# Kernel optimization log

Measured on AMD Instinct MI355X. Metric: run time of the kernel, lower is better.

## Reference

```python
import jax, jax.numpy as jnp
import numpy as np

D_MODEL, N_LEVELS, N_HEADS, N_POINTS = 256, 4, 8, 4
DH = D_MODEL // N_HEADS
SPATIAL = np.array([[92, 92], [46, 46], [23, 23], [12, 12]], dtype=np.int64)
LEVEL_START = np.concatenate([[0], np.cumsum(SPATIAL[:, 0] * SPATIAL[:, 1])[:-1]]).astype(np.int64)
LEN_IN = int((SPATIAL[:, 0] * SPATIAL[:, 1]).sum())  # 11253
B, Q = 2, LEN_IN


def _radial_bias():
    # Matches FlashDeformAttnTorch._reset_parameters sampling_offsets bias init.
    thetas = np.arange(N_HEADS, dtype=np.float32) * (2.0 * np.pi / N_HEADS)
    grid = np.stack([np.cos(thetas), np.sin(thetas)], -1)  # (G,2)
    grid = grid / np.abs(grid).max(-1, keepdims=True)
    grid = np.tile(grid[:, None, None, :], (1, N_LEVELS, N_POINTS, 1)).copy()
    for i in range(N_POINTS):
        grid[:, :, i, :] *= i + 1
    return jnp.asarray(grid.reshape(-1), dtype=jnp.float32)


def setup_inputs() -> dict:
    key = jax.random.key(0)
    ks = jax.random.split(key, 10)
    s = 1.0 / np.sqrt(D_MODEL)
    return {
        "query": jax.random.normal(ks[0], (B, Q, D_MODEL), jnp.float32),
        "reference_points": jax.random.uniform(ks[1], (B, Q, N_LEVELS, 2), jnp.float32),
        "input_flatten": jax.random.normal(ks[2], (B, LEN_IN, D_MODEL), jnp.float32),
        "spatial_shapes": SPATIAL,
        "level_start_index": LEVEL_START,
        "W_off": jax.random.normal(ks[3], (D_MODEL, N_HEADS * N_LEVELS * N_POINTS * 2), jnp.float32) * 0.01,
        "b_off": _radial_bias(),
        "W_attn": jax.random.normal(ks[4], (D_MODEL, N_HEADS * N_LEVELS * N_POINTS), jnp.float32) * 0.01,
        "b_attn": jnp.zeros((N_HEADS * N_LEVELS * N_POINTS,), jnp.float32),
        "W_val": jax.random.normal(ks[5], (D_MODEL, D_MODEL), jnp.float32) * s,
        "b_val": jnp.zeros((D_MODEL,), jnp.float32),
        "W_out": jax.random.normal(ks[6], (D_MODEL, D_MODEL), jnp.float32) * s,
        "b_out": jnp.zeros((D_MODEL,), jnp.float32),
    }


def _forward(query, reference_points, input_flatten, W_off, b_off, W_attn, b_attn,
             W_val, b_val, W_out, b_out, spatial_shapes, level_start_index):
    Bn, Qn, _ = query.shape
    G, L, K, Dh = N_HEADS, N_LEVELS, N_POINTS, DH
    ss = np.asarray(spatial_shapes)
    lsi = np.asarray(level_start_index)

    value = (input_flatten @ W_val + b_val).reshape(Bn, -1, G, Dh)
    offsets = (query @ W_off + b_off).reshape(Bn, Qn, G, L, K, 2)
    logits = (query @ W_attn + b_attn).reshape(Bn, Qn, G, L * K)
    attn = jax.nn.softmax(logits, axis=-1).reshape(Bn, Qn, G, L, K)

    # normalizer stacks (W, H) per level
    normalizer = jnp.asarray(np.stack([ss[:, 1], ss[:, 0]], -1).astype(np.float32))
    loc = reference_points[:, :, None, :, None, :] + offsets / normalizer[None, None, None, :, None, :]
    # loc: (B, Q, G, L, K, 2) with (..., 0)=x, (..., 1)=y in [0,1]

    out = jnp.zeros((Bn, Qn, G, Dh), value.dtype)
    for lvl in range(L):
        H, W = int(ss[lvl, 0]), int(ss[lvl, 1])
        start = int(lsi[lvl])
        vlev = value[:, start:start + H * W].transpose(0, 2, 1, 3)  # (B, G, H*W, Dh)
        h_im = loc[:, :, :, lvl, :, 1] * H - 0.5  # (B, Q, G, K)
        w_im = loc[:, :, :, lvl, :, 0] * W - 0.5
        h0 = jnp.floor(h_im); w0 = jnp.floor(w_im)
        lh = h_im - h0; lw = w_im - w0
        hh = 1.0 - lh; hw = 1.0 - lw
        h0i = h0.astype(jnp.int32); w0i = w0.astype(jnp.int32)

        def corner(hi, wi, vlev=vlev, H=H, W=W):
            m = (hi >= 0) & (hi < H) & (wi >= 0) & (wi < W)
            idx = jnp.clip(hi, 0, H - 1) * W + jnp.clip(wi, 0, W - 1)  # (B,Q,G,K)
            idx_bg = idx.transpose(0, 2, 1, 3).reshape(Bn, G, Qn * K)
            g = jax.vmap(jax.vmap(lambda v, i: v[i]))(vlev, idx_bg)  # (B,G,Q*K,Dh)
            g = g.reshape(Bn, G, Qn, K, Dh).transpose(0, 2, 1, 3, 4)  # (B,Q,G,K,Dh)
            return g * m.transpose(0, 1, 2, 3)[..., None].astype(g.dtype)

        v1 = corner(h0i, w0i)
        v2 = corner(h0i, w0i + 1)
        v3 = corner(h0i + 1, w0i)
        v4 = corner(h0i + 1, w0i + 1)
        sampled = (v1 * (hh * hw)[..., None] + v2 * (hh * lw)[..., None]
                   + v3 * (lh * hw)[..., None] + v4 * (lh * lw)[..., None])
        valid = (h_im > -1) & (w_im > -1) & (h_im < H) & (w_im < W)
        sampled = sampled * valid[..., None].astype(sampled.dtype)
        out = out + (sampled * attn[:, :, :, lvl, :, None]).sum(axis=3)

    out = out.reshape(Bn, Qn, G * Dh)
    return out @ W_out + b_out


def reference(query, reference_points, input_flatten, spatial_shapes, level_start_index,
              W_off, b_off, W_attn, b_attn, W_val, b_val, W_out, b_out):
    return _forward(query, reference_points, input_flatten, W_off, b_off, W_attn, b_attn,
                    W_val, b_val, W_out, b_out, spatial_shapes, level_start_index)
```

## Files before the change

### kernel.cpp

```cpp
#include <hip/hip_runtime.h>
#include <math.h>

#define NQ      11253
#define MTOT    22506
#define MPAD    22528
#define LEN_IN  11253

typedef unsigned short u16;
typedef u16   u16x8 __attribute__((ext_vector_type(8)));
typedef float f32x4 __attribute__((ext_vector_type(4)));

__device__ __forceinline__ u16 f2bf(float x) {
    unsigned u = __float_as_uint(x);
    return (u16)((u + 0x7fffu + ((u >> 16) & 1u)) >> 16);
}
__device__ __forceinline__ float bf2f(u16 h) {
    return __uint_as_float(((unsigned)h) << 16);
}
__device__ __forceinline__ void MFMA(f32x4& d, u16x8 a, u16x8 b) {
    asm("v_mfma_f32_16x16x32_bf16 %0, %1, %2, %0" : "+v"(d) : "v"(a), "v"(b));
}
__device__ __forceinline__ void glds16(const void* g, void* l) {
    __builtin_amdgcn_global_load_lds(
        (const __attribute__((address_space(1))) unsigned int*)g,
        (__attribute__((address_space(3))) unsigned int*)l, 16, 0, 0);
}

__global__ __launch_bounds__(256) void prep_w(
    const float* __restrict__ Wv, const float* __restrict__ Wo,
    const float* __restrict__ Wa, const float* __restrict__ Wu,
    u16* __restrict__ wvh, u16* __restrict__ wolh, u16* __restrict__ wuh)
{
    const int k = blockIdx.x;
    const int t = threadIdx.x;
    wvh[t * 256 + k] = f2bf(Wv[k * 256 + t]);
    wuh[t * 256 + k] = f2bf(Wu[k * 256 + t]);
    wolh[t * 256 + k] = f2bf(Wo[k * 256 + t]);
    if (t < 128) wolh[(256 + t) * 256 + k] = f2bf(Wa[k * 128 + t]);
}

__global__ __launch_bounds__(256) void gemm_s1(
    const float* __restrict__ inputf, const float* __restrict__ query,
    const u16* __restrict__ wvh, const u16* __restrict__ wolh,
    const float* __restrict__ bias_v, const float* __restrict__ bias_o,
    const float* __restrict__ bias_a,
    float* __restrict__ offsets, float* __restrict__ logits,
    u16* __restrict__ valbf)
{
    __shared__ __align__(16) u16 AS0[128 * 64];
    __shared__ __align__(16) u16 BS0[128 * 64];

    const int tid = threadIdx.x;
    const int l = tid & 63, wid = tid >> 6;
    const int wr = wid >> 1, wc = wid & 1;
    const int lr = l & 15;
    const int bm = blockIdx.x * 128;
    const int ny = blockIdx.y;

    const float* A = (ny < 2) ? inputf : query;
    const u16*   B = (ny < 2) ? (wvh + ny * 128 * 256)
                              : (wolh + (ny - 2) * 128 * 256);

    f32x4 acc[4][4];
#pragma unroll
    for (int i = 0; i < 4; ++i)
#pragma unroll
        for (int j = 0; j < 4; ++j) acc[i][j] = (f32x4)0.f;

    for (int k0 = 0; k0 < 256; k0 += 64) {
        {
            const int r = tid >> 1, h = tid & 1;
            const bool ok = (bm + r) < MTOT;
            const float* src = &A[(size_t)(bm + r) * 256 + k0 + h * 32];
            float4 f[8];
#pragma unroll
            for (int c = 0; c < 4; ++c) {
                f[2 * c]     = ok ? *(const float4*)(src + c * 8)     : make_float4(0.f,0.f,0.f,0.f);
                f[2 * c + 1] = ok ? *(const float4*)(src + c * 8 + 4) : make_float4(0.f,0.f,0.f,0.f);
            }
#pragma unroll
            for (int c = 0; c < 4; ++c) {
                const int s = h * 4 + c;
                const float* p = (const float*)&f[2 * c];
                u16x8 hv;
#pragma unroll
                for (int j = 0; j < 8; ++j) hv[j] = f2bf(p[j]);
                *(u16x8*)&AS0[r * 64 + ((s ^ (r & 7)) * 8)] = hv;
            }
        }
#pragma unroll
        for (int j = 0; j < 4; ++j) {
            const int ld = wid * 4 + j;
            const int rn = ld * 8 + (l >> 3);
            const int gs = (l & 7) ^ (l >> 3);
            glds16(B + (size_t)rn * 256 + k0 + gs * 8, &BS0[ld * 512]);
        }
        __syncthreads();

#pragma unroll
        for (int kk = 0; kk < 2; ++kk) {
            const int ks = kk * 4 + (l >> 4);
            u16x8 a0[4], b0[4];
#pragma unroll
            for (int t4 = 0; t4 < 4; ++t4) {
                const int ra = wr * 64 + t4 * 16 + lr;
                const int rb = wc * 64 + t4 * 16 + lr;
                a0[t4] = *(const u16x8*)&AS0[ra * 64 + ((ks ^ (ra & 7)) * 8)];
                b0[t4] = *(const u16x8*)&BS0[rb * 64 + ((ks ^ (rb & 7)) * 8)];
            }
#pragma unroll
            for (int mt = 0; mt < 4; ++mt)
#pragma unroll
                for (int nt = 0; nt < 4; ++nt)
                    MFMA(acc[mt][nt], a0[mt], b0[nt]);
        }
        __syncthreads();
    }

    asm volatile("s_nop 7\n\ts_nop 7");

#pragma unroll
    for (int mt = 0; mt < 4; ++mt)
#pragma unroll
        for (int j = 0; j < 4; ++j) {
            const int m = bm + wr * 64 + mt * 16 + (l >> 4) * 4 + j;
            if (m >= MTOT) continue;
#pragma unroll
            for (int nt = 0; nt < 4; ++nt) {
                const int nl = wc * 64 + nt * 16 + lr;
                const float val = acc[mt][nt][j];
                if (ny < 2) {
                    const int n = ny * 128 + nl;
                    const int bi = (m >= LEN_IN) ? 1 : 0;
                    const int pix = m - bi * LEN_IN;
                    valbf[((size_t)((bi << 3) | (n >> 5)) * LEN_IN + pix) * 32 + (n & 31)]
                        = f2bf(val + bias_v[n]);
                } else {
                    const int n = (ny - 2) * 128 + nl;
                    if (n < 256) offsets[(size_t)m * 256 + n] = val + bias_o[n];
                    else logits[(size_t)m * 128 + (n - 256)] = val + bias_a[n - 256];
                }
            }
        }
}

__global__ __launch_bounds__(256) void gemm_out(
    const u16* __restrict__ Ah, const u16* __restrict__ Bh,
    const float* __restrict__ bias0, float* __restrict__ Cf)
{
    __shared__ __align__(16) u16 AS0[128 * 64];
    __shared__ __align__(16) u16 BS0[128 * 64];

    const int tid = threadIdx.x;
    const int l = tid & 63, wid = tid >> 6;
    const int wr = wid >> 1, wc = wid & 1;
    const int lr = l & 15;
    const int bm = blockIdx.x * 128, bn = blockIdx.y * 128;

    f32x4 acc[4][4];
#pragma unroll
    for (int i = 0; i < 4; ++i)
#pragma unroll
        for (int j = 0; j < 4; ++j) acc[i][j] = (f32x4)0.f;

    for (int k0 = 0; k0 < 256; k0 += 64) {
#pragma unroll
        for (int j = 0; j < 4; ++j) {
            const int ld = wid * 4 + j;
            const int r  = ld * 8 + (l >> 3);
            const int gs = (l & 7) ^ (l >> 3);
            glds16(Ah + (size_t)(bm + r) * 256 + k0 + gs * 8, &AS0[ld * 512]);
            glds16(Bh + (size_t)(bn + r) * 256 + k0 + gs * 8, &BS0[ld * 512]);
        }
        __syncthreads();

#pragma unroll
        for (int kk = 0; kk < 2; ++kk) {
            const int ks = kk * 4 + (l >> 4);
            u16x8 a0[4], b0[4];
#pragma unroll
            for (int t4 = 0; t4 < 4; ++t4) {
                const int ra = wr * 64 + t4 * 16 + lr;
                const int rb = wc * 64 + t4 * 16 + lr;
                a0[t4] = *(const u16x8*)&AS0[ra * 64 + ((ks ^ (ra & 7)) * 8)];
                b0[t4] = *(const u16x8*)&BS0[rb * 64 + ((ks ^ (rb & 7)) * 8)];
            }
#pragma unroll
            for (int mt = 0; mt < 4; ++mt)
#pragma unroll
                for (int nt = 0; nt < 4; ++nt)
                    MFMA(acc[mt][nt], a0[mt], b0[nt]);
        }
        __syncthreads();
    }

    asm volatile("s_nop 7\n\ts_nop 7");

#pragma unroll
    for (int mt = 0; mt < 4; ++mt)
#pragma unroll
        for (int j = 0; j < 4; ++j) {
            const int m = bm + wr * 64 + mt * 16 + (l >> 4) * 4 + j;
            if (m >= MTOT) continue;
#pragma unroll
            for (int nt = 0; nt < 4; ++nt) {
                const int n = bn + wc * 64 + nt * 16 + lr;
                Cf[(size_t)m * 256 + n] = acc[mt][nt][j] + bias0[n];
            }
        }
}

__global__ __launch_bounds__(256) void deform_sample(
    const u16* __restrict__ valbf, const float* __restrict__ offsets,
    const float* __restrict__ logits, const float* __restrict__ refp,
    u16* __restrict__ inner)
{
    const int tid = threadIdx.x;
    const int qi = blockIdx.x * 8 + (tid >> 5);
    if (qi >= MTOT) return;
    const int lq = tid & 31;
    const int g = lq >> 2, d8 = (lq & 3) * 8;
    const int b = (qi >= NQ) ? 1 : 0;

    const float* lg  = logits  + (size_t)qi * 128 + g * 16;
    const float* off = offsets + (size_t)qi * 256 + g * 32;
    const float* ref = refp    + (size_t)qi * 8;
    const u16* vbase = valbf + ((size_t)(b * 8 + g) * LEN_IN) * 32 + d8;

    float w[16];
    float mx = -1e30f;
#pragma unroll
    for (int i = 0; i < 16; ++i) { w[i] = lg[i]; mx = fmaxf(mx, w[i]); }
    float s = 0.f;
#pragma unroll
    for (int i = 0; i < 16; ++i) { w[i] = __expf(w[i] - mx); s += w[i]; }
    const float inv = 1.f / s;

    constexpr int Hs[4] = {92, 46, 23, 12};
    constexpr int Ss[4] = {0, 8464, 10580, 11109};

    float acc[8];
#pragma unroll
    for (int j = 0; j < 8; ++j) acc[j] = 0.f;

#pragma unroll
    for (int l = 0; l < 4; ++l) {
        const int Hn = Hs[l];
        const float Hf = (float)Hn;
        const float rx = ref[l * 2 + 0];
        const float ry = ref[l * 2 + 1];
        const u16* vlev = vbase + (size_t)Ss[l] * 32;

        uint4 cv[16];
        float cw[16];
#pragma unroll
        for (int k = 0; k < 4; ++k) {
            const float ox = off[(l * 4 + k) * 2 + 0];
            const float oy = off[(l * 4 + k) * 2 + 1];
            const float x = (rx + ox / Hf) * Hf - 0.5f;
            const float y = (ry + oy / Hf) * Hf - 0.5f;
            float aw = w[l * 4 + k];
            if (!(y > -1.f && x > -1.f && y < Hf && x < Hf)) aw = 0.f;
            const float h0f = floorf(y), w0f = floorf(x);
            const float lh = y - h0f, lw = x - w0f;
            const float hh = 1.f - lh, hw = 1.f - lw;
            const int h0 = (int)h0f, w0 = (int)w0f;
            const int base = h0 * Hn + w0;
            const bool hv0 = (unsigned)h0 < (unsigned)Hn;
            const bool hv1 = (unsigned)(h0 + 1) < (unsigned)Hn;
            const bool wv0 = (unsigned)w0 < (unsigned)Hn;
            const bool wv1 = (unsigned)(w0 + 1) < (unsigned)Hn;
            const bool v00 = hv0 && wv0, v01 = hv0 && wv1;
            const bool v10 = hv1 && wv0, v11 = hv1 && wv1;
            cw[k * 4 + 0] = v00 ? hh * hw * aw : 0.f;
            cw[k * 4 + 1] = v01 ? hh * lw * aw : 0.f;
            cw[k * 4 + 2] = v10 ? lh * hw * aw : 0.f;
            cw[k * 4 + 3] = v11 ? lh * lw * aw : 0.f;
            cv[k * 4 + 0] = *(const uint4*)(vlev + (size_t)(v00 ? base : 0) * 32);
            cv[k * 4 + 1] = *(const uint4*)(vlev + (size_t)(v01 ? base + 1 : 0) * 32);
            cv[k * 4 + 2] = *(const uint4*)(vlev + (size_t)(v10 ? base + Hn : 0) * 32);
            cv[k * 4 + 3] = *(const uint4*)(vlev + (size_t)(v11 ? base + Hn + 1 : 0) * 32);
        }
#pragma unroll
        for (int i = 0; i < 16; ++i) {
            const float c_ = cw[i];
            const uint4 v = cv[i];
            acc[0] += __uint_as_float(v.x << 16) * c_;
            acc[1] += __uint_as_float(v.x & 0xffff0000u) * c_;
            acc[2] += __uint_as_float(v.y << 16) * c_;
            acc[3] += __uint_as_float(v.y & 0xffff0000u) * c_;
            acc[4] += __uint_as_float(v.z << 16) * c_;
            acc[5] += __uint_as_float(v.z & 0xffff0000u) * c_;
            acc[6] += __uint_as_float(v.w << 16) * c_;
            acc[7] += __uint_as_float(v.w & 0xffff0000u) * c_;
        }
    }

    u16x8 hv;
#pragma unroll
    for (int j = 0; j < 8; ++j) hv[j] = f2bf(acc[j] * inv);
    *(u16x8*)&inner[(size_t)qi * 256 + g * 32 + d8] = hv;
}

extern "C" void kernel_launch(void* const* d_in, const int* in_sizes, int n_in,
                              void* d_out, int out_size, void* d_ws, size_t ws_size,
                              hipStream_t stream)
{
    const float* query  = (const float*)d_in[0];
    const float* refp   = (const float*)d_in[1];
    const float* inputf = (const float*)d_in[2];
    const float* W_off  = (const float*)d_in[5];
    const float* b_off  = (const float*)d_in[6];
    const float* W_att  = (const float*)d_in[7];
    const float* b_att  = (const float*)d_in[8];
    const float* W_val  = (const float*)d_in[9];
    const float* b_val  = (const float*)d_in[10];
    const float* W_out  = (const float*)d_in[11];
    const float* b_out  = (const float*)d_in[12];
    float* out = (float*)d_out;

    char* ws = (char*)d_ws;
    size_t o = 0;
    float* offsets = (float*)(ws + o); o += (size_t)MTOT * 256 * 4;
    float* logits  = (float*)(ws + o); o += (size_t)MTOT * 128 * 4;
    u16*   valbf   = (u16*)  (ws + o); o += (size_t)MTOT * 256 * 2;
    u16*   inner   = (u16*)  (ws + o); o += (size_t)MPAD * 256 * 2;
    u16*   wvh     = (u16*)  (ws + o); o += 256 * 256 * 2;
    u16*   wolh    = (u16*)  (ws + o); o += 384 * 256 * 2;
    u16*   wuh     = (u16*)  (ws + o); o += 256 * 256 * 2;

    dim3 blk(256);

    hipLaunchKernelGGL(prep_w, dim3(256), blk, 0, stream,
                       W_val, W_off, W_att, W_out, wvh, wolh, wuh);

    hipLaunchKernelGGL(gemm_s1, dim3(176, 5), blk, 0, stream,
                       inputf, query, wvh, wolh, b_val, b_off, b_att,
                       offsets, logits, valbf);

    hipLaunchKernelGGL(deform_sample, dim3((MTOT + 7) / 8), blk, 0, stream,
                       valbf, offsets, logits, refp, inner);

    hipLaunchKernelGGL(gemm_out, dim3(176, 2), blk, 0, stream,
                       inner, wuh, b_out, out);
}
```

Measured before the change: 209.6 us.

## Pre-convert activations to bf16 and double-buffer LDS in both GEMMs

A prep pass now converts input_flatten and query to bf16 once, so gemm_s1 can stream the A operand with direct global-to-LDS loads instead of converting fp32 in registers on every k-step. Both GEMMs get two LDS buffers so the next k-tile loads while the current tile is multiplied. This removes the redundant fp32 reads and conversions that were repeated across the five column blocks, at the cost of an extra pass writing and re-reading bf16 copies and twice the shared memory per block. The inner buffer now reuses the ih workspace.

```diff
diff --git a/kernel.cpp b/kernel.cpp
--- a/kernel.cpp
+++ b/kernel.cpp
@@ -26,29 +26,51 @@
         (__attribute__((address_space(3))) unsigned int*)l, 16, 0, 0);
 }
 
-__global__ __launch_bounds__(256) void prep_w(
+__global__ __launch_bounds__(256) void prep(
+    const float* __restrict__ inputf, const float* __restrict__ query,
     const float* __restrict__ Wv, const float* __restrict__ Wo,
     const float* __restrict__ Wa, const float* __restrict__ Wu,
-    u16* __restrict__ wvh, u16* __restrict__ wolh, u16* __restrict__ wuh)
-{
-    const int k = blockIdx.x;
+    u16* __restrict__ ih, u16* __restrict__ qh, u16* __restrict__ wvh,
+    u16* __restrict__ wolh, u16* __restrict__ wuh)
+{
     const int t = threadIdx.x;
-    wvh[t * 256 + k] = f2bf(Wv[k * 256 + t]);
-    wuh[t * 256 + k] = f2bf(Wu[k * 256 + t]);
-    wolh[t * 256 + k] = f2bf(Wo[k * 256 + t]);
-    if (t < 128) wolh[(256 + t) * 256 + k] = f2bf(Wa[k * 128 + t]);
+    if (blockIdx.y == 0) {
+        const int row = blockIdx.x * 8 + (t >> 5);
+        const int col = (t & 31) * 8;
+        const size_t idx = (size_t)row * 256 + col;
+        const bool ok = row < MTOT;
+        float4 a0 = make_float4(0.f,0.f,0.f,0.f), a1 = a0, b0 = a0, b1 = a0;
+        if (ok) {
+            a0 = *(const float4*)&inputf[idx]; a1 = *(const float4*)&inputf[idx + 4];
+            b0 = *(const float4*)&query[idx];  b1 = *(const float4*)&query[idx + 4];
+        }
+        const float av[8] = {a0.x, a0.y, a0.z, a0.w, a1.x, a1.y, a1.z, a1.w};
+        const float bv[8] = {b0.x, b0.y, b0.z, b0.w, b1.x, b1.y, b1.z, b1.w};
+        u16x8 ha, hb;
+#pragma unroll
+        for (int j = 0; j < 8; ++j) { ha[j] = f2bf(av[j]); hb[j] = f2bf(bv[j]); }
+        *(u16x8*)&ih[idx] = ha;
+        *(u16x8*)&qh[idx] = hb;
+    } else {
+        const int k = blockIdx.x;
+        if (k >= 256) return;
+        wvh[t * 256 + k] = f2bf(Wv[k * 256 + t]);
+        wuh[t * 256 + k] = f2bf(Wu[k * 256 + t]);
+        wolh[t * 256 + k] = f2bf(Wo[k * 256 + t]);
+        if (t < 128) wolh[(256 + t) * 256 + k] = f2bf(Wa[k * 128 + t]);
+    }
 }
 
 __global__ __launch_bounds__(256) void gemm_s1(
-    const float* __restrict__ inputf, const float* __restrict__ query,
+    const u16* __restrict__ ih, const u16* __restrict__ qh,
     const u16* __restrict__ wvh, const u16* __restrict__ wolh,
     const float* __restrict__ bias_v, const float* __restrict__ bias_o,
     const float* __restrict__ bias_a,
     float* __restrict__ offsets, float* __restrict__ logits,
     u16* __restrict__ valbf)
 {
-    __shared__ __align__(16) u16 AS0[128 * 64];
-    __shared__ __align__(16) u16 BS0[128 * 64];
+    __shared__ __align__(16) u16 AS[2][128 * 64];
+    __shared__ __align__(16) u16 BS[2][128 * 64];
 
     const int tid = threadIdx.x;
     const int l = tid & 63, wid = tid >> 6;
@@ -57,9 +79,9 @@
     const int bm = blockIdx.x * 128;
     const int ny = blockIdx.y;
 
-    const float* A = (ny < 2) ? inputf : query;
-    const u16*   B = (ny < 2) ? (wvh + ny * 128 * 256)
-                              : (wolh + (ny - 2) * 128 * 256);
+    const u16* A = (ny < 2) ? ih : qh;
+    const u16* B = (ny < 2) ? (wvh + ny * 128 * 256)
+                            : (wolh + (ny - 2) * 128 * 256);
 
     f32x4 acc[4][4];
 #pragma unroll
@@ -67,36 +89,27 @@
 #pragma unroll
         for (int j = 0; j < 4; ++j) acc[i][j] = (f32x4)0.f;
 
-    for (int k0 = 0; k0 < 256; k0 += 64) {
-        {
-            const int r = tid >> 1, h = tid & 1;
-            const bool ok = (bm + r) < MTOT;
-            const float* src = &A[(size_t)(bm + r) * 256 + k0 + h * 32];
-            float4 f[8];
-#pragma unroll
-            for (int c = 0; c < 4; ++c) {
-                f[2 * c]     = ok ? *(const float4*)(src + c * 8)     : make_float4(0.f,0.f,0.f,0.f);
-                f[2 * c + 1] = ok ? *(const float4*)(src + c * 8 + 4) : make_float4(0.f,0.f,0.f,0.f);
-            }
-#pragma unroll
-            for (int c = 0; c < 4; ++c) {
-                const int s = h * 4 + c;
-                const float* p = (const float*)&f[2 * c];
-                u16x8 hv;
-#pragma unroll
-                for (int j = 0; j < 8; ++j) hv[j] = f2bf(p[j]);
-                *(u16x8*)&AS0[r * 64 + ((s ^ (r & 7)) * 8)] = hv;
-            }
-        }
-#pragma unroll
-        for (int j = 0; j < 4; ++j) {
-            const int ld = wid * 4 + j;
-            const int rn = ld * 8 + (l >> 3);
-            const int gs = (l & 7) ^ (l >> 3);
-            glds16(B + (size_t)rn * 256 + k0 + gs * 8, &BS0[ld * 512]);
-        }
-        __syncthreads();
-
+    const int rsub = l >> 3;
+    const int gs = (l & 7) ^ rsub;
+
+#define STAGE(b, k0)                                                          \
+    {                                                                         \
+        _Pragma("unroll")                                                     \
+        for (int j = 0; j < 4; ++j) {                                         \
+            const int ld = wid * 4 + j;                                       \
+            const int r  = ld * 8 + rsub;                                     \
+            glds16(A + (size_t)(bm + r) * 256 + (k0) + gs * 8, &AS[b][ld * 512]); \
+            glds16(B + (size_t)r * 256 + (k0) + gs * 8, &BS[b][ld * 512]);    \
+        }                                                                     \
+    }
+
+    STAGE(0, 0);
+    __syncthreads();
+
+#pragma unroll
+    for (int kt = 0; kt < 4; ++kt) {
+        const int cur = kt & 1;
+        if (kt < 3) STAGE(cur ^ 1, (kt + 1) * 64);
 #pragma unroll
         for (int kk = 0; kk < 2; ++kk) {
             const int ks = kk * 4 + (l >> 4);
@@ -105,8 +118,8 @@
             for (int t4 = 0; t4 < 4; ++t4) {
                 const int ra = wr * 64 + t4 * 16 + lr;
                 const int rb = wc * 64 + t4 * 16 + lr;
-                a0[t4] = *(const u16x8*)&AS0[ra * 64 + ((ks ^ (ra & 7)) * 8)];
-                b0[t4] = *(const u16x8*)&BS0[rb * 64 + ((ks ^ (rb & 7)) * 8)];
+                a0[t4] = *(const u16x8*)&AS[cur][ra * 64 + ((ks ^ (ra & 7)) * 8)];
+                b0[t4] = *(const u16x8*)&BS[cur][rb * 64 + ((ks ^ (rb & 7)) * 8)];
             }
 #pragma unroll
             for (int mt = 0; mt < 4; ++mt)
@@ -116,6 +129,7 @@
         }
         __syncthreads();
     }
+#undef STAGE
 
     asm volatile("s_nop 7\n\ts_nop 7");
 
@@ -148,8 +162,8 @@
     const u16* __restrict__ Ah, const u16* __restrict__ Bh,
     const float* __restrict__ bias0, float* __restrict__ Cf)
 {
-    __shared__ __align__(16) u16 AS0[128 * 64];
-    __shared__ __align__(16) u16 BS0[128 * 64];
+    __shared__ __align__(16) u16 AS[2][128 * 64];
+    __shared__ __align__(16) u16 BS[2][128 * 64];
 
     const int tid = threadIdx.x;
     const int l = tid & 63, wid = tid >> 6;
@@ -163,17 +177,27 @@
 #pragma unroll
         for (int j = 0; j < 4; ++j) acc[i][j] = (f32x4)0.f;
 
-    for (int k0 = 0; k0 < 256; k0 += 64) {
-#pragma unroll
-        for (int j = 0; j < 4; ++j) {
-            const int ld = wid * 4 + j;
-            const int r  = ld * 8 + (l >> 3);
-            const int gs = (l & 7) ^ (l >> 3);
-            glds16(Ah + (size_t)(bm + r) * 256 + k0 + gs * 8, &AS0[ld * 512]);
-            glds16(Bh + (size_t)(bn + r) * 256 + k0 + gs * 8, &BS0[ld * 512]);
-        }
-        __syncthreads();
-
+    const int rsub = l >> 3;
+    const int gs = (l & 7) ^ rsub;
+
+#define STAGE(b, k0)                                                          \
+    {                                                                         \
+        _Pragma("unroll")                                                     \
+        for (int j = 0; j < 4; ++j) {                                         \
+            const int ld = wid * 4 + j;                                       \
+            const int r  = ld * 8 + rsub;                                     \
+            glds16(Ah + (size_t)(bm + r) * 256 + (k0) + gs * 8, &AS[b][ld * 512]); \
+            glds16(Bh + (size_t)(bn + r) * 256 + (k0) + gs * 8, &BS[b][ld * 512]); \
+        }                                                                     \
+    }
+
+    STAGE(0, 0);
+    __syncthreads();
+
+#pragma unroll
+    for (int kt = 0; kt < 4; ++kt) {
+        const int cur = kt & 1;
+        if (kt < 3) STAGE(cur ^ 1, (kt + 1) * 64);
 #pragma unroll
         for (int kk = 0; kk < 2; ++kk) {
             const int ks = kk * 4 + (l >> 4);
@@ -182,8 +206,8 @@
             for (int t4 = 0; t4 < 4; ++t4) {
                 const int ra = wr * 64 + t4 * 16 + lr;
                 const int rb = wc * 64 + t4 * 16 + lr;
-                a0[t4] = *(const u16x8*)&AS0[ra * 64 + ((ks ^ (ra & 7)) * 8)];
-                b0[t4] = *(const u16x8*)&BS0[rb * 64 + ((ks ^ (rb & 7)) * 8)];
+                a0[t4] = *(const u16x8*)&AS[cur][ra * 64 + ((ks ^ (ra & 7)) * 8)];
+                b0[t4] = *(const u16x8*)&BS[cur][rb * 64 + ((ks ^ (rb & 7)) * 8)];
             }
 #pragma unroll
             for (int mt = 0; mt < 4; ++mt)
@@ -193,6 +217,7 @@
         }
         __syncthreads();
     }
+#undef STAGE
 
     asm volatile("s_nop 7\n\ts_nop 7");
 
@@ -324,18 +349,21 @@
     float* offsets = (float*)(ws + o); o += (size_t)MTOT * 256 * 4;
     float* logits  = (float*)(ws + o); o += (size_t)MTOT * 128 * 4;
     u16*   valbf   = (u16*)  (ws + o); o += (size_t)MTOT * 256 * 2;
-    u16*   inner   = (u16*)  (ws + o); o += (size_t)MPAD * 256 * 2;
+    u16*   ih      = (u16*)  (ws + o); o += (size_t)MPAD * 256 * 2;
+    u16*   qh      = (u16*)  (ws + o); o += (size_t)MPAD * 256 * 2;
     u16*   wvh     = (u16*)  (ws + o); o += 256 * 256 * 2;
     u16*   wolh    = (u16*)  (ws + o); o += 384 * 256 * 2;
     u16*   wuh     = (u16*)  (ws + o); o += 256 * 256 * 2;
+    u16*   inner   = ih;
 
     dim3 blk(256);
 
-    hipLaunchKernelGGL(prep_w, dim3(256), blk, 0, stream,
-                       W_val, W_off, W_att, W_out, wvh, wolh, wuh);
+    hipLaunchKernelGGL(prep, dim3(2816, 2), blk, 0, stream,
+                       inputf, query, W_val, W_off, W_att, W_out,
+                       ih, qh, wvh, wolh, wuh);
 
     hipLaunchKernelGGL(gemm_s1, dim3(176, 5), blk, 0, stream,
-                       inputf, query, wvh, wolh, b_val, b_off, b_att,
+                       ih, qh, wvh, wolh, b_val, b_off, b_att,
                        offsets, logits, valbf);
 
     hipLaunchKernelGGL(deform_sample, dim3((MTOT + 7) / 8), blk, 0, stream,
```

New measurement: 203.6 us. 2.8% less time.
